# Kernel optimization log

Hardware: AMD Instinct MI355X
Metric: run time of the kernel (lower is better)

## Reference

```python
import jax, jax.numpy as jnp
import numpy as np

IN_CH = 32
HID = 2 * IN_CH          # 64
MASK_CH = 8 * 27         # 216


def conv3d(x, w, b, replicate_pad):
    # x: [B,C,D,H,W], w: [O,I,kd,kh,kw]
    if replicate_pad:
        x = jnp.pad(x, ((0, 0), (0, 0), (1, 1), (1, 1), (1, 1)), mode='edge')
    y = jax.lax.conv_general_dilated(
        x, w, window_strides=(1, 1, 1), padding='VALID',
        dimension_numbers=('NCDHW', 'OIDHW', 'NCDHW'))
    return y + b[None, :, None, None, None]


def unfold27(x):
    # replicate-padded 3x3x3 neighborhoods -> [B,C,D,H,W,27], n = kd*9+kh*3+kw
    B, C, D, H, W = x.shape
    xp = jnp.pad(x, ((0, 0), (0, 0), (1, 1), (1, 1), (1, 1)), mode='edge')
    patches = [xp[:, :, dz:dz + D, dy:dy + H, dx:dx + W]
               for dz in range(3) for dy in range(3) for dx in range(3)]
    return jnp.stack(patches, axis=-1)


def setup_inputs() -> dict:
    key = jax.random.key(0)
    ks = jax.random.split(key, 6)
    B, C, D, H, W = 1, IN_CH, 48, 48, 48
    x = jax.random.normal(ks[0], (B, C, D, H, W), dtype=jnp.float32)
    features = jax.random.normal(ks[1], (B, IN_CH, D, H, W), dtype=jnp.float32)
    # Conv(in, 2*in, k=3, replicate pad) ; Conv(2*in, 8*27, k=1, zeros pad)
    w1 = jax.random.normal(ks[2], (HID, IN_CH, 3, 3, 3), dtype=jnp.float32) * (1.0 / np.sqrt(IN_CH * 27))
    b1 = jnp.zeros((HID,), dtype=jnp.float32)
    w2 = jax.random.normal(ks[3], (MASK_CH, HID, 1, 1, 1), dtype=jnp.float32) * (1.0 / np.sqrt(HID))
    b2 = jnp.zeros((MASK_CH,), dtype=jnp.float32)
    return {"x": x, "features": features, "w1": w1, "b1": b1, "w2": w2, "b2": b2}


def reference(x, features, w1, b1, w2, b2):
    B, C, D, H, W = x.shape
    # mask network: Conv3 (replicate) -> SiLU -> Conv1 (zeros)
    h = jax.nn.silu(conv3d(features, w1, b1, replicate_pad=True))
    m = conv3d(h, w2, b2, replicate_pad=False)          # [B,216,D,H,W]
    # view(B,1,2,2,2,27,D,H,W).permute(0,1,6,2,7,3,8,4,5) -> [B,D,2,H,2,W,2,27]
    m = m.reshape(B, 2, 2, 2, 27, D, H, W)
    m = jnp.transpose(m, (0, 5, 1, 6, 2, 7, 3, 4))      # b d i h j w k n
    m = jax.nn.softmax(m, axis=-1)
    xu = unfold27(x)                                    # [B,C,D,H,W,27]
    # convex combination: contract over the 27 taps (batched small matmul)
    out = jnp.einsum('bdihjwkn,bcdhwn->bcdihjwk', m, xu)
    return out.reshape(B, C, 2 * D, 2 * H, 2 * W)
```

## Files before the change

### kernel.cpp

```cpp
#include <hip/hip_runtime.h>
#include <math.h>

#define NVOX 110592

typedef _Float16 f16x8 __attribute__((ext_vector_type(8)));
typedef _Float16 f16x4 __attribute__((ext_vector_type(4)));
typedef _Float16 f16x2 __attribute__((ext_vector_type(2)));
typedef float    f32x4 __attribute__((ext_vector_type(4)));

__device__ __forceinline__ void fmas4(float4& a, const float4& xv, float p) {
    a.x = fmaf(xv.x, p, a.x);
    a.y = fmaf(xv.y, p, a.y);
    a.z = fmaf(xv.z, p, a.z);
    a.w = fmaf(xv.w, p, a.w);
}
__device__ __forceinline__ float comp4(const float4& v, int j) {
    return j == 0 ? v.x : (j == 1 ? v.y : (j == 2 ? v.z : v.w));
}

__device__ __forceinline__ int xcd_swizzle(int bx, int nwg) {
    int chunk = nwg >> 3;
    return (bx & 7) * chunk + (bx >> 3);
}

__global__ __launch_bounds__(256) void k_prep(
    const float* __restrict__ feat, const float* __restrict__ x,
    const float* __restrict__ w1, const float* __restrict__ w2,
    _Float16* __restrict__ featT, _Float16* __restrict__ xT,
    _Float16* __restrict__ w1h, _Float16* __restrict__ w2h)
{
    __shared__ _Float16 tile[64 * 36];
    int bx = blockIdx.x;
    int t = threadIdx.x;

    if (bx >= 3456) {
        int e = (bx - 3456) * 256 + t;
        if (e < 64 * 32 * 27) {
            int oc = e / 864;
            int r = e - oc * 864;
            int ci = r / 27;
            int tap = r - ci * 27;
            w1h[oc * 864 + tap * 32 + ci] = (_Float16)w1[e];
        }
        int e2 = e - 55296;
        if (e2 >= 0 && e2 < 224 * 64) {
            int oc = e2 >> 6, k = e2 & 63;
            w2h[e2] = (oc < 216) ? (_Float16)w2[oc * 64 + k] : (_Float16)0.f;
        }
        return;
    }

    int which = bx >= 1728;
    int v0 = (which ? bx - 1728 : bx) * 64;
    const float* s = which ? x : feat;
    _Float16* dt = which ? xT : featT;

    for (int i = t; i < 1024; i += 256) {
        int c2 = i >> 6, dv = i & 63;
        f16x2 v;
        v.x = (_Float16)s[(2 * c2) * NVOX + v0 + dv];
        v.y = (_Float16)s[(2 * c2 + 1) * NVOX + v0 + dv];
        *(f16x2*)(tile + dv * 36 + c2 * 2) = v;
    }
    __syncthreads();
    for (int i = t; i < 512; i += 256) {
        int dv = i >> 3, ch = i & 7;
        f16x4 v = *(const f16x4*)(tile + dv * 36 + ch * 4);
        *(f16x4*)(dt + (v0 + dv) * 32 + ch * 4) = v;
    }
}

__global__ __launch_bounds__(512, 4) void k_main(
    const _Float16* __restrict__ featT, const _Float16* __restrict__ xT,
    const _Float16* __restrict__ w1h, const float* __restrict__ b1,
    const _Float16* __restrict__ w2h, const float* __restrict__ b2,
    float* __restrict__ out)
{
    __shared__ float smem[19752];
    float* mbuf = smem;
    _Float16* X  = (_Float16*)(smem + 10752);
    _Float16* hl = (_Float16*)(smem + 10752);

    int bx = xcd_swizzle(blockIdx.x, gridDim.x);
    int d = bx / 48, hh = bx - d * 48;
    int t = threadIdx.x;

    for (int i = t; i < 1800; i += 512) {
        int col = i >> 2, chunk = i & 3;
        int dzdy = col / 50;
        int px = col - dzdy * 50;
        int dz = dzdy / 3, dy = dzdy - dz * 3;
        int zz = min(max(d + dz - 1, 0), 47);
        int yy = min(max(hh + dy - 1, 0), 47);
        int xx = min(max(px - 1, 0), 47);
        int vox = (zz * 48 + yy) * 48 + xx;
        *(f16x8*)(X + col * 40 + chunk * 8) =
            *(const f16x8*)(featT + vox * 32 + chunk * 8);
    }
    __syncthreads();

    int wid = t >> 6;
    int lane = t & 63;
    int mcol = lane & 15;
    int q = lane >> 4;
    int ocs = wid & 3;

    f32x4 c1a = {0.f, 0.f, 0.f, 0.f};
    f32x4 c1b = {0.f, 0.f, 0.f, 0.f};
    {
        const _Float16* wbase = w1h + (ocs * 16 + mcol) * 864 + q * 8;
#pragma unroll 3
        for (int dzdy = 0; dzdy < 9; ++dzdy) {
            const _Float16* brow = X + (dzdy * 50 + mcol) * 40 + q * 8;
            const _Float16* wrow = wbase + dzdy * 96;
#pragma unroll
            for (int dx = 0; dx < 3; ++dx) {
                f16x8 av = *(const f16x8*)(wrow + dx * 32);
                const _Float16* bb = brow + dx * 40;
                if (wid < 4) {
                    f16x8 b0 = *(const f16x8*)(bb);
                    f16x8 b2v = *(const f16x8*)(bb + 32 * 40);
                    c1a = __builtin_amdgcn_mfma_f32_16x16x32_f16(av, b0, c1a, 0, 0, 0);
                    c1b = __builtin_amdgcn_mfma_f32_16x16x32_f16(av, b2v, c1b, 0, 0, 0);
                } else {
                    f16x8 b1v = *(const f16x8*)(bb + 16 * 40);
                    c1a = __builtin_amdgcn_mfma_f32_16x16x32_f16(av, b1v, c1a, 0, 0, 0);
                }
            }
        }
    }
    __syncthreads();

    {
        float4 bv = ((const float4*)b1)[ocs * 4 + q];
        int pxb0 = (wid < 4) ? 0 : 1;
        int px0 = pxb0 * 16 + mcol;
        f16x4 o; float s;
        s = c1a[0] + bv.x; o.x = (_Float16)(s / (1.f + __expf(-s)));
        s = c1a[1] + bv.y; o.y = (_Float16)(s / (1.f + __expf(-s)));
        s = c1a[2] + bv.z; o.z = (_Float16)(s / (1.f + __expf(-s)));
        s = c1a[3] + bv.w; o.w = (_Float16)(s / (1.f + __expf(-s)));
        *(f16x4*)(hl + px0 * 72 + ocs * 16 + q * 4) = o;
        if (wid < 4) {
            int px1 = 32 + mcol;
            s = c1b[0] + bv.x; o.x = (_Float16)(s / (1.f + __expf(-s)));
            s = c1b[1] + bv.y; o.y = (_Float16)(s / (1.f + __expf(-s)));
            s = c1b[2] + bv.z; o.z = (_Float16)(s / (1.f + __expf(-s)));
            s = c1b[3] + bv.w; o.w = (_Float16)(s / (1.f + __expf(-s)));
            *(f16x4*)(hl + px1 * 72 + ocs * 16 + q * 4) = o;
        }
    }
    __syncthreads();

    for (int tt = wid; tt < 42; tt += 8) {
        int mt = tt / 3, nt = tt - mt * 3;
        float bias[4];
#pragma unroll
        for (int rr = 0; rr < 4; ++rr) {
            int oc = mt * 16 + q * 4 + rr;
            bias[rr] = (oc < 216) ? b2[oc] : 0.f;
        }
        f32x4 acc = {bias[0], bias[1], bias[2], bias[3]};
#pragma unroll
        for (int ks = 0; ks < 2; ++ks) {
            f16x8 av = *(const f16x8*)(w2h + (mt * 16 + mcol) * 64 + ks * 32 + q * 8);
            f16x8 bv = *(const f16x8*)(hl + (nt * 16 + mcol) * 72 + ks * 32 + q * 8);
            acc = __builtin_amdgcn_mfma_f32_16x16x32_f16(av, bv, acc, 0, 0, 0);
        }
        int vox = nt * 16 + mcol;
#pragma unroll
        for (int rr = 0; rr < 4; ++rr) {
            int oc = mt * 16 + q * 4 + rr;
            if (oc < 216) {
                int sub = oc / 27;
                int n = oc - sub * 27;
                mbuf[(sub * 48 + vox) * 28 + n] = acc[rr];
            }
        }
    }
    __syncthreads();

    for (int i = t; i < 1800; i += 512) {
        int col = i >> 2, chunk = i & 3;
        int dzdy = col / 50;
        int px = col - dzdy * 50;
        int dz = dzdy / 3, dy = dzdy - dz * 3;
        int zz = min(max(d + dz - 1, 0), 47);
        int yy = min(max(hh + dy - 1, 0), 47);
        int xx = min(max(px - 1, 0), 47);
        int vox = (zz * 48 + yy) * 48 + xx;
        *(f16x8*)(X + col * 40 + chunk * 8) =
            *(const f16x8*)(xT + vox * 32 + chunk * 8);
    }
    if (t < 384) {
        int sub = t / 48;
        int vox = t - sub * 48;
        float4* p4p = (float4*)(mbuf + (sub * 48 + vox) * 28);
        float4 v[7];
#pragma unroll
        for (int g = 0; g < 7; ++g) v[g] = p4p[g];
        float mx = fmaxf(fmaxf(v[6].x, v[6].y), v[6].z);
#pragma unroll
        for (int g = 0; g < 6; ++g)
            mx = fmaxf(mx, fmaxf(fmaxf(v[g].x, v[g].y), fmaxf(v[g].z, v[g].w)));
        float s = 0.f;
#pragma unroll
        for (int g = 0; g < 7; ++g) {
            v[g].x = __expf(v[g].x - mx);
            v[g].y = __expf(v[g].y - mx);
            v[g].z = __expf(v[g].z - mx);
            v[g].w = __expf(v[g].w - mx);
        }
        v[6].w = 0.f;
#pragma unroll
        for (int g = 0; g < 7; ++g) s += v[g].x + v[g].y + v[g].z + v[g].w;
        float inv = 1.f / s;
#pragma unroll
        for (int g = 0; g < 7; ++g) {
            v[g].x *= inv; v[g].y *= inv; v[g].z *= inv; v[g].w *= inv;
            p4p[g] = v[g];
        }
    }
    __syncthreads();

    float4* smem4 = (float4*)smem;
    int u = t & 255;
    int half = t >> 8;
    int w0 = half * 24;
    int tx = u & 7, ty = u >> 3;
    int cq = ty & 7, sp = ty >> 3;
    float4 acc[2][3];
#pragma unroll
    for (int s = 0; s < 2; ++s)
#pragma unroll
        for (int wi = 0; wi < 3; ++wi)
            acc[s][wi] = make_float4(0.f, 0.f, 0.f, 0.f);

#pragma unroll
    for (int g = 0; g < 7; ++g) {
        float4 p4[2][3];
#pragma unroll
        for (int s = 0; s < 2; ++s)
#pragma unroll
            for (int wi = 0; wi < 3; ++wi)
                p4[s][wi] = smem4[((sp * 2 + s) * 48 + w0 + tx + wi * 8) * 7 + g];
#pragma unroll
        for (int j = 0; j < 4; ++j) {
            int n = g * 4 + j;
            if (n < 27) {
                int dz = n / 9;
                int rem = n - dz * 9;
                int dy = rem / 3, dx = rem - dy * 3;
#pragma unroll
                for (int wi = 0; wi < 3; ++wi) {
                    int col = (dz * 3 + dy) * 50 + w0 + tx + wi * 8 + dx;
                    f16x4 xr = *(const f16x4*)(X + col * 40 + cq * 4);
                    float4 xv = make_float4((float)xr.x, (float)xr.y,
                                            (float)xr.z, (float)xr.w);
                    fmas4(acc[0][wi], xv, comp4(p4[0][wi], j));
                    fmas4(acc[1][wi], xv, comp4(p4[1][wi], j));
                }
            }
        }
    }

    int i_ = sp >> 1, j_ = sp & 1;
    int rowz = 2 * d + i_;
    int rowy = 2 * hh + j_;
#pragma unroll
    for (int wi = 0; wi < 3; ++wi) {
        int wg = w0 + tx + wi * 8;
#pragma unroll
        for (int cc = 0; cc < 4; ++cc) {
            int c = cq * 4 + cc;
            float2 v;
            v.x = comp4(acc[0][wi], cc);
            v.y = comp4(acc[1][wi], cc);
            *(float2*)(out + (((size_t)c * 96 + rowz) * 96 + rowy) * 96 + 2 * wg) = v;
        }
    }
}

extern "C" void kernel_launch(void* const* d_in, const int* in_sizes, int n_in,
                              void* d_out, int out_size, void* d_ws, size_t ws_size,
                              hipStream_t stream) {
    const float* x    = (const float*)d_in[0];
    const float* feat = (const float*)d_in[1];
    const float* w1   = (const float*)d_in[2];
    const float* b1   = (const float*)d_in[3];
    const float* w2   = (const float*)d_in[4];
    const float* b2   = (const float*)d_in[5];
    float* out = (float*)d_out;

    _Float16* w1h   = (_Float16*)d_ws;
    _Float16* w2h   = (_Float16*)((char*)d_ws + 110592);
    _Float16* featT = (_Float16*)((char*)d_ws + 139264);
    _Float16* xT    = (_Float16*)((char*)d_ws + 7217152);

    k_prep<<<3728, 256, 0, stream>>>(feat, x, w1, w2, featT, xT, w1h, w2h);
    k_main<<<2304, 512, 0, stream>>>(featT, xT, w1h, b1, w2h, b2, out);
}
```

Measured before the change: 247.6 us.

## Read x taps from global fp32 channel-last buffer and remap conv1 waves

The x tensor is now transposed to a channel-last fp32 buffer rather than fp16, and the convex-combination stage reads its 27 neighbour taps straight from global memory instead of first staging a halo tile in LDS. Each of 384 threads handles all 8 sub-voxels for one (w, channel-quad) pair, so each x value loaded is reused across 8 mask weights. Conv1 is remapped so 6 waves each compute 32 output channels for one 16-pixel block, sharing the B operand across two MFMAs. This removes one LDS fill and an fp16 rounding of x, at the cost of twice the workspace traffic for x and more global loads served by L1/L2.

```diff
diff --git a/kernel.cpp b/kernel.cpp
--- a/kernel.cpp
+++ b/kernel.cpp
@@ -8,12 +8,6 @@
 typedef _Float16 f16x2 __attribute__((ext_vector_type(2)));
 typedef float    f32x4 __attribute__((ext_vector_type(4)));
 
-__device__ __forceinline__ void fmas4(float4& a, const float4& xv, float p) {
-    a.x = fmaf(xv.x, p, a.x);
-    a.y = fmaf(xv.y, p, a.y);
-    a.z = fmaf(xv.z, p, a.z);
-    a.w = fmaf(xv.w, p, a.w);
-}
 __device__ __forceinline__ float comp4(const float4& v, int j) {
     return j == 0 ? v.x : (j == 1 ? v.y : (j == 2 ? v.z : v.w));
 }
@@ -26,10 +20,10 @@
 __global__ __launch_bounds__(256) void k_prep(
     const float* __restrict__ feat, const float* __restrict__ x,
     const float* __restrict__ w1, const float* __restrict__ w2,
-    _Float16* __restrict__ featT, _Float16* __restrict__ xT,
+    _Float16* __restrict__ featT, float* __restrict__ xT32,
     _Float16* __restrict__ w1h, _Float16* __restrict__ w2h)
 {
-    __shared__ _Float16 tile[64 * 36];
+    __shared__ float tileb[64 * 34];
     int bx = blockIdx.x;
     int t = threadIdx.x;
 
@@ -50,28 +44,45 @@
         return;
     }
 
-    int which = bx >= 1728;
-    int v0 = (which ? bx - 1728 : bx) * 64;
-    const float* s = which ? x : feat;
-    _Float16* dt = which ? xT : featT;
-
-    for (int i = t; i < 1024; i += 256) {
-        int c2 = i >> 6, dv = i & 63;
-        f16x2 v;
-        v.x = (_Float16)s[(2 * c2) * NVOX + v0 + dv];
-        v.y = (_Float16)s[(2 * c2 + 1) * NVOX + v0 + dv];
-        *(f16x2*)(tile + dv * 36 + c2 * 2) = v;
-    }
-    __syncthreads();
-    for (int i = t; i < 512; i += 256) {
-        int dv = i >> 3, ch = i & 7;
-        f16x4 v = *(const f16x4*)(tile + dv * 36 + ch * 4);
-        *(f16x4*)(dt + (v0 + dv) * 32 + ch * 4) = v;
+    if (bx < 1728) {
+        _Float16* tile = (_Float16*)tileb;
+        int v0 = bx * 64;
+        for (int i = t; i < 1024; i += 256) {
+            int c2 = i >> 6, dv = i & 63;
+            f16x2 v;
+            v.x = (_Float16)feat[(2 * c2) * NVOX + v0 + dv];
+            v.y = (_Float16)feat[(2 * c2 + 1) * NVOX + v0 + dv];
+            *(f16x2*)(tile + dv * 36 + c2 * 2) = v;
+        }
+        __syncthreads();
+        for (int i = t; i < 512; i += 256) {
+            int dv = i >> 3, ch = i & 7;
+            f16x4 v = *(const f16x4*)(tile + dv * 36 + ch * 4);
+            *(f16x4*)(featT + (v0 + dv) * 32 + ch * 4) = v;
+        }
+        return;
+    }
+
+    {
+        int v0 = (bx - 1728) * 64;
+        for (int i = t; i < 1024; i += 256) {
+            int c2 = i >> 6, dv = i & 63;
+            float2 v;
+            v.x = x[(2 * c2) * NVOX + v0 + dv];
+            v.y = x[(2 * c2 + 1) * NVOX + v0 + dv];
+            *(float2*)(tileb + dv * 34 + c2 * 2) = v;
+        }
+        __syncthreads();
+        for (int i = t; i < 1024; i += 256) {
+            int dv = i >> 4, ch = i & 15;
+            float2 v = *(const float2*)(tileb + dv * 34 + ch * 2);
+            *(float2*)(xT32 + (size_t)(v0 + dv) * 32 + ch * 2) = v;
+        }
     }
 }
 
 __global__ __launch_bounds__(512, 4) void k_main(
-    const _Float16* __restrict__ featT, const _Float16* __restrict__ xT,
+    const _Float16* __restrict__ featT, const float* __restrict__ xT32,
     const _Float16* __restrict__ w1h, const float* __restrict__ b1,
     const _Float16* __restrict__ w2h, const float* __restrict__ b2,
     float* __restrict__ out)
@@ -103,52 +114,46 @@
     int lane = t & 63;
     int mcol = lane & 15;
     int q = lane >> 4;
-    int ocs = wid & 3;
 
     f32x4 c1a = {0.f, 0.f, 0.f, 0.f};
     f32x4 c1b = {0.f, 0.f, 0.f, 0.f};
-    {
-        const _Float16* wbase = w1h + (ocs * 16 + mcol) * 864 + q * 8;
+    int pxb = wid >> 1;
+    int och = wid & 1;
+    if (wid < 6) {
+        const _Float16* wb0 = w1h + (och * 32 + mcol) * 864 + q * 8;
+        const _Float16* wb1 = wb0 + 16 * 864;
 #pragma unroll 3
         for (int dzdy = 0; dzdy < 9; ++dzdy) {
-            const _Float16* brow = X + (dzdy * 50 + mcol) * 40 + q * 8;
-            const _Float16* wrow = wbase + dzdy * 96;
+            const _Float16* brow = X + (dzdy * 50 + pxb * 16 + mcol) * 40 + q * 8;
+            const _Float16* wr0 = wb0 + dzdy * 96;
+            const _Float16* wr1 = wb1 + dzdy * 96;
 #pragma unroll
             for (int dx = 0; dx < 3; ++dx) {
-                f16x8 av = *(const f16x8*)(wrow + dx * 32);
-                const _Float16* bb = brow + dx * 40;
-                if (wid < 4) {
-                    f16x8 b0 = *(const f16x8*)(bb);
-                    f16x8 b2v = *(const f16x8*)(bb + 32 * 40);
-                    c1a = __builtin_amdgcn_mfma_f32_16x16x32_f16(av, b0, c1a, 0, 0, 0);
-                    c1b = __builtin_amdgcn_mfma_f32_16x16x32_f16(av, b2v, c1b, 0, 0, 0);
-                } else {
-                    f16x8 b1v = *(const f16x8*)(bb + 16 * 40);
-                    c1a = __builtin_amdgcn_mfma_f32_16x16x32_f16(av, b1v, c1a, 0, 0, 0);
-                }
+                f16x8 bv = *(const f16x8*)(brow + dx * 40);
+                f16x8 a0 = *(const f16x8*)(wr0 + dx * 32);
+                f16x8 a1 = *(const f16x8*)(wr1 + dx * 32);
+                c1a = __builtin_amdgcn_mfma_f32_16x16x32_f16(a0, bv, c1a, 0, 0, 0);
+                c1b = __builtin_amdgcn_mfma_f32_16x16x32_f16(a1, bv, c1b, 0, 0, 0);
             }
         }
     }
     __syncthreads();
 
-    {
-        float4 bv = ((const float4*)b1)[ocs * 4 + q];
-        int pxb0 = (wid < 4) ? 0 : 1;
-        int px0 = pxb0 * 16 + mcol;
+    if (wid < 6) {
+        int pxv = pxb * 16 + mcol;
+        float4 bva = ((const float4*)b1)[(och * 2) * 4 + q];
+        float4 bvb = ((const float4*)b1)[(och * 2 + 1) * 4 + q];
         f16x4 o; float s;
-        s = c1a[0] + bv.x; o.x = (_Float16)(s / (1.f + __expf(-s)));
-        s = c1a[1] + bv.y; o.y = (_Float16)(s / (1.f + __expf(-s)));
-        s = c1a[2] + bv.z; o.z = (_Float16)(s / (1.f + __expf(-s)));
-        s = c1a[3] + bv.w; o.w = (_Float16)(s / (1.f + __expf(-s)));
-        *(f16x4*)(hl + px0 * 72 + ocs * 16 + q * 4) = o;
-        if (wid < 4) {
-            int px1 = 32 + mcol;
-            s = c1b[0] + bv.x; o.x = (_Float16)(s / (1.f + __expf(-s)));
-            s = c1b[1] + bv.y; o.y = (_Float16)(s / (1.f + __expf(-s)));
-            s = c1b[2] + bv.z; o.z = (_Float16)(s / (1.f + __expf(-s)));
-            s = c1b[3] + bv.w; o.w = (_Float16)(s / (1.f + __expf(-s)));
-            *(f16x4*)(hl + px1 * 72 + ocs * 16 + q * 4) = o;
-        }
+        s = c1a[0] + bva.x; o.x = (_Float16)(s / (1.f + __expf(-s)));
+        s = c1a[1] + bva.y; o.y = (_Float16)(s / (1.f + __expf(-s)));
+        s = c1a[2] + bva.z; o.z = (_Float16)(s / (1.f + __expf(-s)));
+        s = c1a[3] + bva.w; o.w = (_Float16)(s / (1.f + __expf(-s)));
+        *(f16x4*)(hl + pxv * 72 + och * 32 + q * 4) = o;
+        s = c1b[0] + bvb.x; o.x = (_Float16)(s / (1.f + __expf(-s)));
+        s = c1b[1] + bvb.y; o.y = (_Float16)(s / (1.f + __expf(-s)));
+        s = c1b[2] + bvb.z; o.z = (_Float16)(s / (1.f + __expf(-s)));
+        s = c1b[3] + bvb.w; o.w = (_Float16)(s / (1.f + __expf(-s)));
+        *(f16x4*)(hl + pxv * 72 + och * 32 + 16 + q * 4) = o;
     }
     __syncthreads();
 
@@ -180,18 +185,6 @@
     }
     __syncthreads();
 
-    for (int i = t; i < 1800; i += 512) {
-        int col = i >> 2, chunk = i & 3;
-        int dzdy = col / 50;
-        int px = col - dzdy * 50;
-        int dz = dzdy / 3, dy = dzdy - dz * 3;
-        int zz = min(max(d + dz - 1, 0), 47);
-        int yy = min(max(hh + dy - 1, 0), 47);
-        int xx = min(max(px - 1, 0), 47);
-        int vox = (zz * 48 + yy) * 48 + xx;
-        *(f16x8*)(X + col * 40 + chunk * 8) =
-            *(const f16x8*)(xT + vox * 32 + chunk * 8);
-    }
     if (t < 384) {
         int sub = t / 48;
         int vox = t - sub * 48;
@@ -223,60 +216,71 @@
     }
     __syncthreads();
 
-    float4* smem4 = (float4*)smem;
-    int u = t & 255;
-    int half = t >> 8;
-    int w0 = half * 24;
-    int tx = u & 7, ty = u >> 3;
-    int cq = ty & 7, sp = ty >> 3;
-    float4 acc[2][3];
-#pragma unroll
-    for (int s = 0; s < 2; ++s)
-#pragma unroll
-        for (int wi = 0; wi < 3; ++wi)
-            acc[s][wi] = make_float4(0.f, 0.f, 0.f, 0.f);
-
-#pragma unroll
-    for (int g = 0; g < 7; ++g) {
-        float4 p4[2][3];
-#pragma unroll
-        for (int s = 0; s < 2; ++s)
-#pragma unroll
-            for (int wi = 0; wi < 3; ++wi)
-                p4[s][wi] = smem4[((sp * 2 + s) * 48 + w0 + tx + wi * 8) * 7 + g];
-#pragma unroll
-        for (int j = 0; j < 4; ++j) {
-            int n = g * 4 + j;
-            if (n < 27) {
-                int dz = n / 9;
-                int rem = n - dz * 9;
-                int dy = rem / 3, dx = rem - dy * 3;
-#pragma unroll
-                for (int wi = 0; wi < 3; ++wi) {
-                    int col = (dz * 3 + dy) * 50 + w0 + tx + wi * 8 + dx;
-                    f16x4 xr = *(const f16x4*)(X + col * 40 + cq * 4);
-                    float4 xv = make_float4((float)xr.x, (float)xr.y,
-                                            (float)xr.z, (float)xr.w);
-                    fmas4(acc[0][wi], xv, comp4(p4[0][wi], j));
-                    fmas4(acc[1][wi], xv, comp4(p4[1][wi], j));
+    if (t < 384) {
+        int cq = t & 7;
+        int tx = (t >> 3) & 7;
+        int half = (t >> 6) & 1;
+        int wig = t >> 7;
+        int w = half * 24 + wig * 8 + tx;
+
+        int rb[9];
+#pragma unroll
+        for (int r = 0; r < 9; ++r) {
+            int dz = r / 3, dy = r - (r / 3) * 3;
+            int zz = min(max(d + dz - 1, 0), 47);
+            int yy = min(max(hh + dy - 1, 0), 47);
+            rb[r] = (zz * 48 + yy) * 48;
+        }
+        int xs0 = max(w - 1, 0), xs2 = min(w + 1, 47);
+
+        float acc[8][4];
+#pragma unroll
+        for (int sub = 0; sub < 8; ++sub)
+#pragma unroll
+            for (int cc = 0; cc < 4; ++cc) acc[sub][cc] = 0.f;
+
+        const float4* smem4 = (const float4*)smem;
+#pragma unroll
+        for (int g = 0; g < 7; ++g) {
+            float4 p[8];
+#pragma unroll
+            for (int sub = 0; sub < 8; ++sub)
+                p[sub] = smem4[(sub * 48 + w) * 7 + g];
+#pragma unroll
+            for (int j = 0; j < 4; ++j) {
+                int n = g * 4 + j;
+                if (n < 27) {
+                    int r = n / 3;
+                    int dx = n - r * 3;
+                    int xx = (dx == 0) ? xs0 : ((dx == 1) ? w : xs2);
+                    float4 xv = *(const float4*)(xT32 +
+                                  (size_t)(rb[r] + xx) * 32 + cq * 4);
+#pragma unroll
+                    for (int sub = 0; sub < 8; ++sub) {
+                        float pv = comp4(p[sub], j);
+                        acc[sub][0] = fmaf(xv.x, pv, acc[sub][0]);
+                        acc[sub][1] = fmaf(xv.y, pv, acc[sub][1]);
+                        acc[sub][2] = fmaf(xv.z, pv, acc[sub][2]);
+                        acc[sub][3] = fmaf(xv.w, pv, acc[sub][3]);
+                    }
                 }
             }
         }
-    }
-
-    int i_ = sp >> 1, j_ = sp & 1;
-    int rowz = 2 * d + i_;
-    int rowy = 2 * hh + j_;
-#pragma unroll
-    for (int wi = 0; wi < 3; ++wi) {
-        int wg = w0 + tx + wi * 8;
-#pragma unroll
-        for (int cc = 0; cc < 4; ++cc) {
-            int c = cq * 4 + cc;
-            float2 v;
-            v.x = comp4(acc[0][wi], cc);
-            v.y = comp4(acc[1][wi], cc);
-            *(float2*)(out + (((size_t)c * 96 + rowz) * 96 + rowy) * 96 + 2 * wg) = v;
+
+#pragma unroll
+        for (int ij = 0; ij < 4; ++ij) {
+            int i_ = ij >> 1, j_ = ij & 1;
+            int rowz = 2 * d + i_;
+            int rowy = 2 * hh + j_;
+            int s0 = ij * 2;
+#pragma unroll
+            for (int cc = 0; cc < 4; ++cc) {
+                int c = cq * 4 + cc;
+                float2 v;
+                v.x = acc[s0][cc];
+                v.y = acc[s0 + 1][cc];
+                *(float2*)(out + (((size_t)c * 96 + rowz) * 96 + rowy) * 96 + 2 * w) = v;
+            }
         }
     }
 }
@@ -295,8 +299,8 @@
     _Float16* w1h   = (_Float16*)d_ws;
     _Float16* w2h   = (_Float16*)((char*)d_ws + 110592);
     _Float16* featT = (_Float16*)((char*)d_ws + 139264);
-    _Float16* xT    = (_Float16*)((char*)d_ws + 7217152);
-
-    k_prep<<<3728, 256, 0, stream>>>(feat, x, w1, w2, featT, xT, w1h, w2h);
-    k_main<<<2304, 512, 0, stream>>>(featT, xT, w1h, b1, w2h, b2, out);
-}
+    float*    xT32  = (float*)((char*)d_ws + 7217152);
+
+    k_prep<<<3728, 256, 0, stream>>>(feat, x, w1, w2, featT, xT32, w1h, w2h);
+    k_main<<<2304, 512, 0, stream>>>(featT, xT32, w1h, b1, w2h, b2, out);
+}
```

Result: slower. 278.0 us (+12.3%).

## Read x neighborhoods directly from global instead of staging in LDS, shrink LDS

Applied to the files above, without the earlier changes.

The x-tile staging into shared memory is removed, and the convex-combination stage now loads f16x4 neighbors of x directly from global (L1/L2-cached) memory with replicate clamping. The shared buffer is re-laid out so the mask buffer sits after the conv-staging region, which cuts LDS use. Launch bounds are raised to target more resident blocks. Each tap now costs a global load rather than an LDS read, in exchange for less LDS traffic and higher occupancy. The accumulator loop is restructured per wi to lower register pressure.

```diff
diff --git a/kernel.cpp b/kernel.cpp
--- a/kernel.cpp
+++ b/kernel.cpp
@@ -70,16 +70,16 @@
     }
 }
 
-__global__ __launch_bounds__(512, 4) void k_main(
+__global__ __launch_bounds__(512, 6) void k_main(
     const _Float16* __restrict__ featT, const _Float16* __restrict__ xT,
     const _Float16* __restrict__ w1h, const float* __restrict__ b1,
     const _Float16* __restrict__ w2h, const float* __restrict__ b2,
     float* __restrict__ out)
 {
-    __shared__ float smem[19752];
-    float* mbuf = smem;
-    _Float16* X  = (_Float16*)(smem + 10752);
-    _Float16* hl = (_Float16*)(smem + 10752);
+    __shared__ float smem[12480];
+    _Float16* X  = (_Float16*)smem;
+    _Float16* hl = (_Float16*)smem;
+    float* mbuf  = smem + 1728;
 
     int bx = xcd_swizzle(blockIdx.x, gridDim.x);
     int d = bx / 48, hh = bx - d * 48;
@@ -180,18 +180,6 @@
     }
     __syncthreads();
 
-    for (int i = t; i < 1800; i += 512) {
-        int col = i >> 2, chunk = i & 3;
-        int dzdy = col / 50;
-        int px = col - dzdy * 50;
-        int dz = dzdy / 3, dy = dzdy - dz * 3;
-        int zz = min(max(d + dz - 1, 0), 47);
-        int yy = min(max(hh + dy - 1, 0), 47);
-        int xx = min(max(px - 1, 0), 47);
-        int vox = (zz * 48 + yy) * 48 + xx;
-        *(f16x8*)(X + col * 40 + chunk * 8) =
-            *(const f16x8*)(xT + vox * 32 + chunk * 8);
-    }
     if (t < 384) {
         int sub = t / 48;
         int vox = t - sub * 48;
@@ -223,60 +211,60 @@
     }
     __syncthreads();
 
-    float4* smem4 = (float4*)smem;
-    int u = t & 255;
-    int half = t >> 8;
-    int w0 = half * 24;
-    int tx = u & 7, ty = u >> 3;
-    int cq = ty & 7, sp = ty >> 3;
-    float4 acc[2][3];
-#pragma unroll
-    for (int s = 0; s < 2; ++s)
-#pragma unroll
-        for (int wi = 0; wi < 3; ++wi)
-            acc[s][wi] = make_float4(0.f, 0.f, 0.f, 0.f);
-
-#pragma unroll
-    for (int g = 0; g < 7; ++g) {
-        float4 p4[2][3];
-#pragma unroll
-        for (int s = 0; s < 2; ++s)
-#pragma unroll
-            for (int wi = 0; wi < 3; ++wi)
-                p4[s][wi] = smem4[((sp * 2 + s) * 48 + w0 + tx + wi * 8) * 7 + g];
-#pragma unroll
-        for (int j = 0; j < 4; ++j) {
-            int n = g * 4 + j;
-            if (n < 27) {
-                int dz = n / 9;
-                int rem = n - dz * 9;
-                int dy = rem / 3, dx = rem - dy * 3;
-#pragma unroll
-                for (int wi = 0; wi < 3; ++wi) {
-                    int col = (dz * 3 + dy) * 50 + w0 + tx + wi * 8 + dx;
-                    f16x4 xr = *(const f16x4*)(X + col * 40 + cq * 4);
-                    float4 xv = make_float4((float)xr.x, (float)xr.y,
-                                            (float)xr.z, (float)xr.w);
-                    fmas4(acc[0][wi], xv, comp4(p4[0][wi], j));
-                    fmas4(acc[1][wi], xv, comp4(p4[1][wi], j));
+    {
+        const float4* m4 = (const float4*)mbuf;
+        int u = t & 255;
+        int half = t >> 8;
+        int w0 = half * 24;
+        int tx = u & 7, ty = u >> 3;
+        int cq = ty & 7, sp = ty >> 3;
+
+        int rb[9];
+#pragma unroll
+        for (int r = 0; r < 9; ++r) {
+            int dz = r / 3, dy = r - (r / 3) * 3;
+            int zz = min(max(d + dz - 1, 0), 47);
+            int yy = min(max(hh + dy - 1, 0), 47);
+            rb[r] = (zz * 48 + yy) * 48;
+        }
+        int i_ = sp >> 1, j_ = sp & 1;
+        int rowz = 2 * d + i_;
+        int rowy = 2 * hh + j_;
+
+#pragma unroll
+        for (int wi = 0; wi < 3; ++wi) {
+            int w_ = w0 + tx + wi * 8;
+            int xm = max(w_ - 1, 0), xp = min(w_ + 1, 47);
+            float4 a0 = make_float4(0.f, 0.f, 0.f, 0.f);
+            float4 a1 = make_float4(0.f, 0.f, 0.f, 0.f);
+#pragma unroll
+            for (int g = 0; g < 7; ++g) {
+                float4 p0 = m4[((sp * 2 + 0) * 48 + w_) * 7 + g];
+                float4 p1 = m4[((sp * 2 + 1) * 48 + w_) * 7 + g];
+#pragma unroll
+                for (int j = 0; j < 4; ++j) {
+                    int n = g * 4 + j;
+                    if (n < 27) {
+                        int r = n / 3;
+                        int dx = n - r * 3;
+                        int xx = (dx == 0) ? xm : ((dx == 1) ? w_ : xp);
+                        f16x4 xr = *(const f16x4*)(xT +
+                                      (size_t)(rb[r] + xx) * 32 + cq * 4);
+                        float4 xv = make_float4((float)xr.x, (float)xr.y,
+                                                (float)xr.z, (float)xr.w);
+                        fmas4(a0, xv, comp4(p0, j));
+                        fmas4(a1, xv, comp4(p1, j));
+                    }
                 }
             }
-        }
-    }
-
-    int i_ = sp >> 1, j_ = sp & 1;
-    int rowz = 2 * d + i_;
-    int rowy = 2 * hh + j_;
-#pragma unroll
-    for (int wi = 0; wi < 3; ++wi) {
-        int wg = w0 + tx + wi * 8;
-#pragma unroll
-        for (int cc = 0; cc < 4; ++cc) {
-            int c = cq * 4 + cc;
-            float2 v;
-            v.x = comp4(acc[0][wi], cc);
-            v.y = comp4(acc[1][wi], cc);
-            *(float2*)(out + (((size_t)c * 96 + rowz) * 96 + rowy) * 96 + 2 * wg) = v;
+#pragma unroll
+            for (int cc = 0; cc < 4; ++cc) {
+                int c = cq * 4 + cc;
+                float2 v;
+                v.x = comp4(a0, cc);
+                v.y = comp4(a1, cc);
+                *(float2*)(out + (((size_t)c * 96 + rowz) * 96 + rowy) * 96 + 2 * w_) = v;
+            }
         }
     }
 }
```

New measurement: 374.9 us. +51.4%, slower.

## Shrink LDS by storing softmax weights as fp16 and overlapping buffers

Applied to the files above, without the earlier changes.

Shared memory is repacked so the fp32 mask buffer overlaps the staging area, and the softmax probabilities are written back as fp16 into a compact buffer reused alongside the x tile with a tighter 36-element stride. The LDS footprint drops from about 79KB to about 54KB, which is meant to let more workgroups reside per CU and to halve the bytes read for probabilities in the combine loop. This costs an extra barrier and fp16 rounding of the softmax weights. It also keeps the softmax values in registers across a sync.

```diff
diff --git a/kernel.cpp b/kernel.cpp
--- a/kernel.cpp
+++ b/kernel.cpp
@@ -76,10 +76,12 @@
     const _Float16* __restrict__ w2h, const float* __restrict__ b2,
     float* __restrict__ out)
 {
-    __shared__ float smem[19752];
-    float* mbuf = smem;
-    _Float16* X  = (_Float16*)(smem + 10752);
-    _Float16* hl = (_Float16*)(smem + 10752);
+    __shared__ float smem[13476];
+    _Float16* X  = (_Float16*)smem;
+    _Float16* hl = (_Float16*)smem;
+    float* mbuf  = smem + 1728;
+    _Float16* pb = (_Float16*)smem;
+    _Float16* xs = (_Float16*)smem + 10752;
 
     int bx = xcd_swizzle(blockIdx.x, gridDim.x);
     int d = bx / 48, hh = bx - d * 48;
@@ -180,6 +182,43 @@
     }
     __syncthreads();
 
+    float4 v[7];
+    if (t < 384) {
+        const float4* p4p = (const float4*)(mbuf + t * 28);
+#pragma unroll
+        for (int g = 0; g < 7; ++g) v[g] = p4p[g];
+        float mx = fmaxf(fmaxf(v[6].x, v[6].y), v[6].z);
+#pragma unroll
+        for (int g = 0; g < 6; ++g)
+            mx = fmaxf(mx, fmaxf(fmaxf(v[g].x, v[g].y), fmaxf(v[g].z, v[g].w)));
+        float s = 0.f;
+#pragma unroll
+        for (int g = 0; g < 7; ++g) {
+            v[g].x = __expf(v[g].x - mx);
+            v[g].y = __expf(v[g].y - mx);
+            v[g].z = __expf(v[g].z - mx);
+            v[g].w = __expf(v[g].w - mx);
+        }
+        v[6].w = 0.f;
+#pragma unroll
+        for (int g = 0; g < 7; ++g) s += v[g].x + v[g].y + v[g].z + v[g].w;
+        float inv = 1.f / s;
+#pragma unroll
+        for (int g = 0; g < 7; ++g) {
+            v[g].x *= inv; v[g].y *= inv; v[g].z *= inv; v[g].w *= inv;
+        }
+    }
+    __syncthreads();
+
+    if (t < 384) {
+#pragma unroll
+        for (int g = 0; g < 7; ++g) {
+            f16x4 pv;
+            pv.x = (_Float16)v[g].x; pv.y = (_Float16)v[g].y;
+            pv.z = (_Float16)v[g].z; pv.w = (_Float16)v[g].w;
+            *(f16x4*)(pb + t * 28 + g * 4) = pv;
+        }
+    }
     for (int i = t; i < 1800; i += 512) {
         int col = i >> 2, chunk = i & 3;
         int dzdy = col / 50;
@@ -189,94 +228,70 @@
         int yy = min(max(hh + dy - 1, 0), 47);
         int xx = min(max(px - 1, 0), 47);
         int vox = (zz * 48 + yy) * 48 + xx;
-        *(f16x8*)(X + col * 40 + chunk * 8) =
+        *(f16x8*)(xs + col * 36 + chunk * 8) =
             *(const f16x8*)(xT + vox * 32 + chunk * 8);
     }
-    if (t < 384) {
-        int sub = t / 48;
-        int vox = t - sub * 48;
-        float4* p4p = (float4*)(mbuf + (sub * 48 + vox) * 28);
-        float4 v[7];
-#pragma unroll
-        for (int g = 0; g < 7; ++g) v[g] = p4p[g];
-        float mx = fmaxf(fmaxf(v[6].x, v[6].y), v[6].z);
-#pragma unroll
-        for (int g = 0; g < 6; ++g)
-            mx = fmaxf(mx, fmaxf(fmaxf(v[g].x, v[g].y), fmaxf(v[g].z, v[g].w)));
-        float s = 0.f;
+    __syncthreads();
+
+    {
+        int u = t & 255;
+        int half = t >> 8;
+        int w0 = half * 24;
+        int tx = u & 7, ty = u >> 3;
+        int cq = ty & 7, sp = ty >> 3;
+        float4 acc[2][3];
+#pragma unroll
+        for (int s = 0; s < 2; ++s)
+#pragma unroll
+            for (int wi = 0; wi < 3; ++wi)
+                acc[s][wi] = make_float4(0.f, 0.f, 0.f, 0.f);
+
 #pragma unroll
         for (int g = 0; g < 7; ++g) {
-            v[g].x = __expf(v[g].x - mx);
-            v[g].y = __expf(v[g].y - mx);
-            v[g].z = __expf(v[g].z - mx);
-            v[g].w = __expf(v[g].w - mx);
-        }
-        v[6].w = 0.f;
-#pragma unroll
-        for (int g = 0; g < 7; ++g) s += v[g].x + v[g].y + v[g].z + v[g].w;
-        float inv = 1.f / s;
-#pragma unroll
-        for (int g = 0; g < 7; ++g) {
-            v[g].x *= inv; v[g].y *= inv; v[g].z *= inv; v[g].w *= inv;
-            p4p[g] = v[g];
-        }
-    }
-    __syncthreads();
-
-    float4* smem4 = (float4*)smem;
-    int u = t & 255;
-    int half = t >> 8;
-    int w0 = half * 24;
-    int tx = u & 7, ty = u >> 3;
-    int cq = ty & 7, sp = ty >> 3;
-    float4 acc[2][3];
-#pragma unroll
-    for (int s = 0; s < 2; ++s)
-#pragma unroll
-        for (int wi = 0; wi < 3; ++wi)
-            acc[s][wi] = make_float4(0.f, 0.f, 0.f, 0.f);
-
-#pragma unroll
-    for (int g = 0; g < 7; ++g) {
-        float4 p4[2][3];
-#pragma unroll
-        for (int s = 0; s < 2; ++s)
-#pragma unroll
-            for (int wi = 0; wi < 3; ++wi)
-                p4[s][wi] = smem4[((sp * 2 + s) * 48 + w0 + tx + wi * 8) * 7 + g];
-#pragma unroll
-        for (int j = 0; j < 4; ++j) {
-            int n = g * 4 + j;
-            if (n < 27) {
-                int dz = n / 9;
-                int rem = n - dz * 9;
-                int dy = rem / 3, dx = rem - dy * 3;
+            float4 p4[2][3];
+#pragma unroll
+            for (int s = 0; s < 2; ++s)
 #pragma unroll
                 for (int wi = 0; wi < 3; ++wi) {
-                    int col = (dz * 3 + dy) * 50 + w0 + tx + wi * 8 + dx;
-                    f16x4 xr = *(const f16x4*)(X + col * 40 + cq * 4);
-                    float4 xv = make_float4((float)xr.x, (float)xr.y,
-                                            (float)xr.z, (float)xr.w);
-                    fmas4(acc[0][wi], xv, comp4(p4[0][wi], j));
-                    fmas4(acc[1][wi], xv, comp4(p4[1][wi], j));
+                    f16x4 pr = *(const f16x4*)(pb +
+                        ((sp * 2 + s) * 48 + w0 + tx + wi * 8) * 28 + g * 4);
+                    p4[s][wi] = make_float4((float)pr.x, (float)pr.y,
+                                            (float)pr.z, (float)pr.w);
+                }
+#pragma unroll
+            for (int j = 0; j < 4; ++j) {
+                int n = g * 4 + j;
+                if (n < 27) {
+                    int dz = n / 9;
+                    int rem = n - dz * 9;
+                    int dy = rem / 3, dx = rem - dy * 3;
+#pragma unroll
+                    for (int wi = 0; wi < 3; ++wi) {
+                        int col = (dz * 3 + dy) * 50 + w0 + tx + wi * 8 + dx;
+                        f16x4 xr = *(const f16x4*)(xs + col * 36 + cq * 4);
+                        float4 xv = make_float4((float)xr.x, (float)xr.y,
+                                                (float)xr.z, (float)xr.w);
+                        fmas4(acc[0][wi], xv, comp4(p4[0][wi], j));
+                        fmas4(acc[1][wi], xv, comp4(p4[1][wi], j));
+                    }
                 }
             }
         }
-    }
-
-    int i_ = sp >> 1, j_ = sp & 1;
-    int rowz = 2 * d + i_;
-    int rowy = 2 * hh + j_;
-#pragma unroll
-    for (int wi = 0; wi < 3; ++wi) {
-        int wg = w0 + tx + wi * 8;
-#pragma unroll
-        for (int cc = 0; cc < 4; ++cc) {
-            int c = cq * 4 + cc;
-            float2 v;
-            v.x = comp4(acc[0][wi], cc);
-            v.y = comp4(acc[1][wi], cc);
-            *(float2*)(out + (((size_t)c * 96 + rowz) * 96 + rowy) * 96 + 2 * wg) = v;
+
+        int i_ = sp >> 1, j_ = sp & 1;
+        int rowz = 2 * d + i_;
+        int rowy = 2 * hh + j_;
+#pragma unroll
+        for (int wi = 0; wi < 3; ++wi) {
+            int wg = w0 + tx + wi * 8;
+#pragma unroll
+            for (int cc = 0; cc < 4; ++cc) {
+                int c = cq * 4 + cc;
+                float2 vv;
+                vv.x = comp4(acc[0][wi], cc);
+                vv.y = comp4(acc[1][wi], cc);
+                *(float2*)(out + (((size_t)c * 96 + rowz) * 96 + rowy) * 96 + 2 * wg) = vv;
+            }
         }
     }
 }
```

New measurement: 262.1 us. +5.9%, slower.
